# Optimization experiments

Measured on AMD Instinct MI355X. Metric: run time of the kernel, lower is better.

Reference implementation:

```python
import jax, jax.numpy as jnp
import numpy as np

# TT ranks: source list [1,7,7,7,1] interpreted as r_0..r_4 with wraparound r_5 = r_0 = 1
RANKS = [1, 7, 7, 7, 1, 1]
LAYERS = [
    ([7, 4, 4, 4, 7], [8, 8, 8, 8, 4]),   # 3136 -> 16384
    ([8, 8, 8, 8, 4], [8, 8, 8, 4, 4]),   # 16384 -> 8192
    ([8, 8, 8, 4, 4], [8, 8, 4, 4, 4]),   # 8192 -> 4096
    ([8, 8, 4, 4, 4], [8, 4, 4, 4, 4]),   # 4096 -> 2048
    ([8, 4, 4, 4, 4], [10, 1, 1, 1, 1]),  # 2048 -> 10 (out_modes padded with 1s)
]
BATCH = 8192


def tt_linear(x, cores, bias):
    # x: [B, in_features]; cores[i]: [r_i, m_i, n_i, r_{i+1}]
    B = x.shape[0]
    t = x.reshape(B, -1, 1, 1)  # [B, M_remaining, N_done, r]
    for G in cores:
        r0, m, n, r1 = G.shape
        rest = t.shape[1] // m
        t = t.reshape(B, m, rest, t.shape[2], r0)
        # contract current input mode m and incoming rank r0 with the core
        t = jnp.einsum('bmsnp,pmoq->bsnoq', t, G)  # [B, rest, N_done, n, r1]
        t = t.reshape(B, rest, -1, r1)
    return t.reshape(B, -1) + bias  # [B, out_features]


def setup_inputs() -> dict:
    key = jax.random.key(0)
    keys = jax.random.split(key, 32)
    inp = {"x": jax.random.normal(keys[0], (BATCH, 3136), jnp.float32)}
    ki = 1
    for li, (im, om) in enumerate(LAYERS, start=1):
        for ci in range(5):
            shape = (RANKS[ci], im[ci], om[ci], RANKS[ci + 1])
            scale = 1.0 / np.sqrt(im[ci] * RANKS[ci])
            inp[f"l{li}_core{ci}"] = jax.random.normal(keys[ki], shape, jnp.float32) * scale
            ki += 1
        inp[f"l{li}_bias"] = jnp.zeros((int(np.prod(om)),), jnp.float32)
    return inp


def reference(x,
              l1_core0, l1_core1, l1_core2, l1_core3, l1_core4, l1_bias,
              l2_core0, l2_core1, l2_core2, l2_core3, l2_core4, l2_bias,
              l3_core0, l3_core1, l3_core2, l3_core3, l3_core4, l3_bias,
              l4_core0, l4_core1, l4_core2, l4_core3, l4_core4, l4_bias,
              l5_core0, l5_core1, l5_core2, l5_core3, l5_core4, l5_bias):
    h = jax.nn.relu(tt_linear(x, [l1_core0, l1_core1, l1_core2, l1_core3, l1_core4], l1_bias))
    h = jax.nn.relu(tt_linear(h, [l2_core0, l2_core1, l2_core2, l2_core3, l2_core4], l2_bias))
    h = jax.nn.relu(tt_linear(h, [l3_core0, l3_core1, l3_core2, l3_core3, l3_core4], l3_bias))
    h = jax.nn.relu(tt_linear(h, [l4_core0, l4_core1, l4_core2, l4_core3, l4_core4], l4_bias))
    logits = tt_linear(h, [l5_core0, l5_core1, l5_core2, l5_core3, l5_core4], l5_bias)
    return jax.nn.softmax(logits, axis=1)
```

## Files before the change

### kernel.cpp

```cpp
#include <hip/hip_runtime.h>
#include <stdint.h>
#include <stddef.h>

typedef _Float16 f16;
typedef _Float16 f16x8 __attribute__((ext_vector_type(8)));
typedef float    f32x4 __attribute__((ext_vector_type(4)));

#define NB 8192

struct Ptrs {
  const float *G0[5], *G1[5], *G2[5], *G3[5], *bias[5];
  float *T01[5], *T23[5], *biasr[5];
  f16   *WHt[5];
};

__global__ void prep1_kernel(Ptrs p) {
  constexpr int IM[5][5] = {{7,4,4,4,7},{8,8,8,8,4},{8,8,8,4,4},{8,8,4,4,4},{8,4,4,4,4}};
  constexpr int OM[5][5] = {{8,8,8,8,4},{8,8,8,4,4},{8,8,4,4,4},{8,4,4,4,4},{10,1,1,1,1}};
  const int job = blockIdx.x;
  const int tid = threadIdx.x;
  if (job < 5) {
    const int L = job;
    const int m1=IM[L][1], n0=OM[L][0], n1=OM[L][1];
    const int n01 = n0*n1;
    const int cnt = IM[L][0]*m1*n01*7;
    const float* G0 = p.G0[L]; const float* G1 = p.G1[L];
    float* T = p.T01[L];
    for (int e = tid; e < cnt; e += blockDim.x) {
      const int r2  = e % 7;
      const int j01 = (e/7) % n01;
      const int i01 = e / (7*n01);
      const int i0 = i01/m1, i1 = i01 - i0*m1;
      const int j0 = j01/n1, j1 = j01 - j0*n1;
      float s = 0.f;
      for (int r1 = 0; r1 < 7; ++r1)
        s += G0[(i0*n0 + j0)*7 + r1] * G1[((r1*m1 + i1)*n1 + j1)*7 + r2];
      T[e] = s;
    }
  } else if (job < 10) {
    const int L = job - 5;
    const int m2=IM[L][2], m3=IM[L][3], n2=OM[L][2], n3=OM[L][3];
    const int n23 = n2*n3;
    const int cnt = m2*m3*n23*7;
    const float* G2 = p.G2[L]; const float* G3 = p.G3[L];
    float* T = p.T23[L];
    for (int e = tid; e < cnt; e += blockDim.x) {
      const int r2  = e % 7;
      const int j23 = (e/7) % n23;
      const int i23 = e / (7*n23);
      const int i2 = i23/m3, i3 = i23 - i2*m3;
      const int j2 = j23/n3, j3 = j23 - j2*n3;
      float s = 0.f;
      for (int r3 = 0; r3 < 7; ++r3)
        s += G2[((r2*m2 + i2)*n2 + j2)*7 + r3] * G3[(r3*m3 + i3)*n3 + j3];
      T[e] = s;
    }
  } else {
    const int L = job - 10;
    constexpr int OUTF[5] = {16384, 8192, 4096, 2048, 10};
    constexpr int N4[5]   = {4,4,4,4,1};
    const int of = OUTF[L], n4 = N4[L], outH = of / n4;
    const float* b = p.bias[L];
    float* br = p.biasr[L];
    for (int e = tid; e < of; e += blockDim.x) {
      const int j4 = e / outH, jH = e - j4*outH;
      br[e] = b[jH*n4 + j4];
    }
  }
}

__global__ void prep2_kernel(Ptrs p) {
  constexpr int INH[5]  = {448, 4096, 2048, 1024, 512};
  constexpr int M23[5]  = {16, 64, 32, 16, 16};
  constexpr int N23[5]  = {64, 32, 16, 16, 1};
  constexpr int N01[5]  = {64, 64, 64, 32, 10};
  constexpr int BASE[6] = {0, 1835008, 10223616, 12320768, 12845056, 12850176};
  const int total = BASE[5];
  for (int e = blockIdx.x*blockDim.x + threadIdx.x; e < total;
       e += gridDim.x*blockDim.x) {
    int L = 0;
    while (L < 4 && e >= BASE[L+1]) ++L;
    const int le = e - BASE[L];
    const int iH = le % INH[L];
    const int jH = le / INH[L];
    const int i01 = iH / M23[L], i23 = iH - i01*M23[L];
    const int j01 = jH / N23[L], j23 = jH - j01*N23[L];
    const float* a = p.T01[L] + (i01*N01[L] + j01)*7;
    const float* b = p.T23[L] + (i23*N23[L] + j23)*7;
    float s = 0.f;
#pragma unroll
    for (int r = 0; r < 7; ++r) s += a[r]*b[r];
    p.WHt[L][le] = (f16)s;
  }
}

__global__ void stagea_x(const float* __restrict__ x, const float* __restrict__ g4,
                         f16* __restrict__ u, int BC) {
  const int idx = blockIdx.x*blockDim.x + threadIdx.x;
  if (idx >= BC*448) return;
  const int b = idx / 448, c = idx - b*448;
  const float* xr = x + (size_t)b*3136 + c*7;
  float v[7];
#pragma unroll
  for (int i = 0; i < 7; ++i) v[i] = xr[i];
#pragma unroll
  for (int j = 0; j < 4; ++j) {
    float s = 0.f;
#pragma unroll
    for (int i = 0; i < 7; ++i) s += v[i]*g4[i*4+j];
    u[(size_t)(b*4+j)*448 + c] = (f16)s;
  }
}

__global__ void __launch_bounds__(512, 2)
gemm256(const f16* __restrict__ A, const f16* __restrict__ Bt,
        f16* __restrict__ U, const float* __restrict__ biasr,
        const float* __restrict__ g4n,
        int N, int K, int n4n)
{
  __shared__ f16 Ls[2][2][256*64];

  const int tid  = threadIdx.x;
  const int wid  = tid >> 6, lane = tid & 63;
  const int wr   = wid >> 2, wc = wid & 3;
  const int l15  = lane & 15, l4 = lane >> 4, lm = l15 & 7;

  const int nwg = gridDim.x;
  int wg = blockIdx.x;
  if ((nwg & 7) == 0) wg = (wg & 7) * (nwg >> 3) + (wg >> 3);
  const int Nt = N >> 8;
  const int bx = wg / Nt, by = wg - bx * Nt;
  const int m0 = bx << 8, n0 = by << 8;

  const int rr   = tid >> 3;
  const int cs8  = (((tid & 7) ^ (rr & 7)) << 3);
  const int dst0 = tid << 3;

  const int cz0 = ((l4 ^ lm)) << 3;
  const int cz1 = ((4 + l4) ^ lm) << 3;
  const int ax0 = ((wr << 7) + l15) * 64 + cz0;
  const int ax1 = ((wr << 7) + l15) * 64 + cz1;
  const int bx0 = ((wc << 6) + l15) * 64 + cz0;
  const int bx1 = ((wc << 6) + l15) * 64 + cz1;

  f32x4 acc[8][4] = {};
  f16x8 af0[8], bf0[4], af1[8], bf1[4];

  auto stage = [&](int buf, int kt) {
    const f16* gA = A + (size_t)m0 * K + kt;
    const f16* gB = Bt + (size_t)n0 * K + kt;
    f16* dA = &Ls[buf][0][0];
    f16* dB = &Ls[buf][1][0];
#pragma unroll
    for (int q = 0; q < 4; ++q)
      __builtin_amdgcn_global_load_lds(
          (const __attribute__((address_space(1))) void*)(gA + (size_t)(q*64 + rr)*K + cs8),
          (__attribute__((address_space(3))) void*)(dA + q*4096 + dst0), 16, 0, 0);
#pragma unroll
    for (int q = 0; q < 4; ++q)
      __builtin_amdgcn_global_load_lds(
          (const __attribute__((address_space(1))) void*)(gB + (size_t)(q*64 + rr)*K + cs8),
          (__attribute__((address_space(3))) void*)(dB + q*4096 + dst0), 16, 0, 0);
  };

  stage(0, 0);
  asm volatile("s_waitcnt vmcnt(0)" ::: "memory");
  __builtin_amdgcn_s_barrier();
#pragma unroll
  for (int n = 0; n < 4; ++n) bf0[n] = *(const f16x8*)(&Ls[0][1][0] + bx0 + n*1024);
#pragma unroll
  for (int m = 0; m < 8; ++m) af0[m] = *(const f16x8*)(&Ls[0][0][0] + ax0 + m*1024);

  const int nt = K >> 6;
  for (int t = 0; t < nt - 1; ++t) {
    const int cur = t & 1;
    stage(cur ^ 1, (t + 1) << 6);
    __builtin_amdgcn_sched_barrier(0);
    {
      const f16* As = &Ls[cur][0][0];
      const f16* Bs = &Ls[cur][1][0];
#pragma unroll
      for (int n = 0; n < 4; ++n) bf1[n] = *(const f16x8*)(Bs + bx1 + n*1024);
#pragma unroll
      for (int m = 0; m < 8; ++m) af1[m] = *(const f16x8*)(As + ax1 + m*1024);
    }
    __builtin_amdgcn_sched_barrier(0);
    __builtin_amdgcn_s_setprio(1);
#pragma unroll
    for (int m = 0; m < 8; ++m)
#pragma unroll
      for (int n = 0; n < 4; ++n)
        acc[m][n] = __builtin_amdgcn_mfma_f32_16x16x32_f16(af0[m], bf0[n], acc[m][n], 0, 0, 0);
    __builtin_amdgcn_s_setprio(0);
    __builtin_amdgcn_sched_barrier(0);
    asm volatile("s_waitcnt vmcnt(0)" ::: "memory");
    __builtin_amdgcn_s_barrier();
    __builtin_amdgcn_sched_barrier(0);
    {
      const f16* As = &Ls[cur ^ 1][0][0];
      const f16* Bs = &Ls[cur ^ 1][1][0];
#pragma unroll
      for (int n = 0; n < 4; ++n) bf0[n] = *(const f16x8*)(Bs + bx0 + n*1024);
#pragma unroll
      for (int m = 0; m < 8; ++m) af0[m] = *(const f16x8*)(As + ax0 + m*1024);
    }
    __builtin_amdgcn_sched_barrier(0);
    __builtin_amdgcn_s_setprio(1);
#pragma unroll
    for (int m = 0; m < 8; ++m)
#pragma unroll
      for (int n = 0; n < 4; ++n)
        acc[m][n] = __builtin_amdgcn_mfma_f32_16x16x32_f16(af1[m], bf1[n], acc[m][n], 0, 0, 0);
    __builtin_amdgcn_s_setprio(0);
  }
  {
    const int cur = (nt - 1) & 1;
    const f16* As = &Ls[cur][0][0];
    const f16* Bs = &Ls[cur][1][0];
#pragma unroll
    for (int n = 0; n < 4; ++n) bf1[n] = *(const f16x8*)(Bs + bx1 + n*1024);
#pragma unroll
    for (int m = 0; m < 8; ++m) af1[m] = *(const f16x8*)(As + ax1 + m*1024);
    __builtin_amdgcn_s_setprio(1);
#pragma unroll
    for (int m = 0; m < 8; ++m)
#pragma unroll
      for (int n = 0; n < 4; ++n)
        acc[m][n] = __builtin_amdgcn_mfma_f32_16x16x32_f16(af0[m], bf0[n], acc[m][n], 0, 0, 0);
#pragma unroll
    for (int m = 0; m < 8; ++m)
#pragma unroll
      for (int n = 0; n < 4; ++n)
        acc[m][n] = __builtin_amdgcn_mfma_f32_16x16x32_f16(af1[m], bf1[n], acc[m][n], 0, 0, 0);
    __builtin_amdgcn_s_setprio(0);
  }

#pragma unroll
  for (int m = 0; m < 8; ++m) {
    const int rb = m0 + (wr << 7) + (m << 4) + (l4 << 2);
    const int b  = rb >> 2;
#pragma unroll
    for (int n = 0; n < 4; ++n) {
      const int col = n0 + (wc << 6) + (n << 4) + l15;
      float v[4];
#pragma unroll
      for (int r = 0; r < 4; ++r)
        v[r] = fmaxf(acc[m][n][r] + biasr[(size_t)r * N + col], 0.f);
      if (n4n == 4) {
#pragma unroll
        for (int j = 0; j < 4; ++j) {
          float s = v[0]*g4n[j] + v[1]*g4n[4+j] + v[2]*g4n[8+j] + v[3]*g4n[12+j];
          U[(size_t)(b*4 + j) * N + col] = (f16)s;
        }
      } else {
        float s = v[0]*g4n[0] + v[1]*g4n[1] + v[2]*g4n[2] + v[3]*g4n[3];
        U[(size_t)b * N + col] = (f16)s;
      }
    }
  }
}

__global__ void __launch_bounds__(256, 2)
gemm_fused(const f16* __restrict__ A, const f16* __restrict__ Bt,
           f16* __restrict__ U, const float* __restrict__ biasr,
           const float* __restrict__ g4n,
           int N, int K, int n4n)
{
  __shared__ f16 Ls[2][2][128*64];

  const int tid  = threadIdx.x;
  const int wid  = tid >> 6, lane = tid & 63;
  const int wr   = wid >> 1, wc = wid & 1;
  const int l15  = lane & 15, l4 = lane >> 4, lm = l15 & 7;

  const int nwg = gridDim.x;
  int wg = blockIdx.x;
  if ((nwg & 7) == 0) wg = (wg & 7) * (nwg >> 3) + (wg >> 3);
  const int Nt = N >> 7;
  const int bx = wg / Nt, by = wg - bx * Nt;
  const int m0 = bx << 7, n0 = by << 7;

  const int rr   = tid >> 3;
  const int cs8  = (((tid & 7) ^ (rr & 7)) << 3);
  const int dst0 = wid << 9;

  int axoff[2], bxoff[2];
#pragma unroll
  for (int h = 0; h < 2; ++h) {
    const int cz = (((h << 2) + l4) ^ lm) << 3;
    axoff[h] = ((wr << 6) + l15) * 64 + cz;
    bxoff[h] = ((wc << 6) + l15) * 64 + cz;
  }

  f32x4 acc[4][4] = {};

  auto stage = [&](int buf, int kt) {
    const f16* gA = A + (size_t)m0 * K + kt;
    const f16* gB = Bt + (size_t)n0 * K + kt;
    f16* dA = &Ls[buf][0][0];
    f16* dB = &Ls[buf][1][0];
#pragma unroll
    for (int q = 0; q < 4; ++q)
      __builtin_amdgcn_global_load_lds(
          (const __attribute__((address_space(1))) void*)(gA + (size_t)(q*32 + rr)*K + cs8),
          (__attribute__((address_space(3))) void*)(dA + q*2048 + dst0), 16, 0, 0);
#pragma unroll
    for (int q = 0; q < 4; ++q)
      __builtin_amdgcn_global_load_lds(
          (const __attribute__((address_space(1))) void*)(gB + (size_t)(q*32 + rr)*K + cs8),
          (__attribute__((address_space(3))) void*)(dB + q*2048 + dst0), 16, 0, 0);
  };

  stage(0, 0);
  __syncthreads();
  const int nt = K >> 6;
  int cur = 0;
  for (int t = 0; t < nt; ++t) {
    if (t + 1 < nt) stage(cur ^ 1, (t + 1) << 6);
    __builtin_amdgcn_sched_barrier(0);
    const f16* As = &Ls[cur][0][0];
    const f16* Bs = &Ls[cur][1][0];
#pragma unroll
    for (int h = 0; h < 2; ++h) {
      f16x8 af[4], bf[4];
#pragma unroll
      for (int n = 0; n < 4; ++n) bf[n] = *(const f16x8*)(Bs + bxoff[h] + n*1024);
#pragma unroll
      for (int m = 0; m < 4; ++m) af[m] = *(const f16x8*)(As + axoff[h] + m*1024);
      __builtin_amdgcn_s_setprio(1);
#pragma unroll
      for (int m = 0; m < 4; ++m)
#pragma unroll
        for (int n = 0; n < 4; ++n)
          acc[m][n] = __builtin_amdgcn_mfma_f32_16x16x32_f16(af[m], bf[n], acc[m][n], 0, 0, 0);
      __builtin_amdgcn_s_setprio(0);
    }
    __syncthreads();
    cur ^= 1;
  }

#pragma unroll
  for (int m = 0; m < 4; ++m) {
    const int rb = m0 + (wr << 6) + (m << 4) + (l4 << 2);
    const int b  = rb >> 2;
#pragma unroll
    for (int n = 0; n < 4; ++n) {
      const int col = n0 + (wc << 6) + (n << 4) + l15;
      float v[4];
#pragma unroll
      for (int r = 0; r < 4; ++r)
        v[r] = fmaxf(acc[m][n][r] + biasr[(size_t)r * N + col], 0.f);
      if (n4n == 4) {
#pragma unroll
        for (int j = 0; j < 4; ++j) {
          float s = v[0]*g4n[j] + v[1]*g4n[4+j] + v[2]*g4n[8+j] + v[3]*g4n[12+j];
          U[(size_t)(b*4 + j) * N + col] = (f16)s;
        }
      } else {
        float s = v[0]*g4n[0] + v[1]*g4n[1] + v[2]*g4n[2] + v[3]*g4n[3];
        U[(size_t)b * N + col] = (f16)s;
      }
    }
  }
}

__global__ void l5_softmax(const f16* __restrict__ u, const f16* __restrict__ Wt,
                           const float* __restrict__ bias, float* __restrict__ out)
{
  const int wid = threadIdx.x >> 6, lane = threadIdx.x & 63;
  const int row = blockIdx.x*4 + wid;
  float acc[10] = {};
  const f16* ur = u + (size_t)row*512;
#pragma unroll
  for (int t = 0; t < 8; ++t) {
    const float a = (float)ur[t*64 + lane];
#pragma unroll
    for (int j = 0; j < 10; ++j)
      acc[j] += a * (float)Wt[j*512 + t*64 + lane];
  }
#pragma unroll
  for (int j = 0; j < 10; ++j) {
#pragma unroll
    for (int s = 32; s; s >>= 1) acc[j] += __shfl_xor(acc[j], s);
    acc[j] += bias[j];
  }
  float mx = acc[0];
#pragma unroll
  for (int j = 1; j < 10; ++j) mx = fmaxf(mx, acc[j]);
  float sum = 0.f;
#pragma unroll
  for (int j = 0; j < 10; ++j) { acc[j] = __expf(acc[j]-mx); sum += acc[j]; }
  const float inv = 1.f / sum;
  if (lane < 10) out[(size_t)row*10 + lane] = acc[lane]*inv;
}

extern "C" void kernel_launch(void* const* d_in, const int* in_sizes, int n_in,
                              void* d_out, int out_size, void* d_ws, size_t ws_size,
                              hipStream_t stream) {
  (void)in_sizes; (void)n_in; (void)out_size;
  const float* x = (const float*)d_in[0];
  Ptrs p;
  const float* G4[5];
  for (int L = 0; L < 5; ++L) {
    p.G0[L]   = (const float*)d_in[1 + L*6 + 0];
    p.G1[L]   = (const float*)d_in[1 + L*6 + 1];
    p.G2[L]   = (const float*)d_in[1 + L*6 + 2];
    p.G3[L]   = (const float*)d_in[1 + L*6 + 3];
    G4[L]     = (const float*)d_in[1 + L*6 + 4];
    p.bias[L] = (const float*)d_in[1 + L*6 + 5];
  }

  uintptr_t w = (uintptr_t)d_ws;
  auto alloc = [&](size_t bytes) {
    uintptr_t r = w; w += (bytes + 255) & ~(size_t)255; return (void*)r;
  };
  constexpr int  t01sz[5] = {12544, 28672, 28672, 14336, 2240};
  constexpr int  t23sz[5] = {7168, 14336, 3584, 1792, 112};
  constexpr int  brsz[5]  = {16384, 8192, 4096, 2048, 10};
  constexpr long whsz[5]  = {448L*4096, 4096L*2048, 2048L*1024, 1024L*512, 512L*10};
  for (int L = 0; L < 5; ++L) p.T01[L]   = (float*)alloc((size_t)t01sz[L]*4);
  for (int L = 0; L < 5; ++L) p.T23[L]   = (float*)alloc((size_t)t23sz[L]*4);
  for (int L = 0; L < 5; ++L) p.biasr[L] = (float*)alloc((size_t)brsz[L]*4);
  for (int L = 0; L < 5; ++L) p.WHt[L]   = (f16*)alloc((size_t)whsz[L]*2);
  const size_t fixedBytes = (size_t)(w - (uintptr_t)d_ws);

  int BC = 0;
  for (int c = NB; c >= 64; c >>= 1)
    if (fixedBytes + (size_t)c * (16384 + 32768) <= ws_size) { BC = c; break; }
  if (!BC) return;
  f16* bufA = (f16*)alloc((size_t)BC*16384);
  f16* bufB = (f16*)alloc((size_t)BC*32768);

  prep1_kernel<<<15, 256, 0, stream>>>(p);
  prep2_kernel<<<4096, 256, 0, stream>>>(p);

  const int nch = NB / BC;
  const int M   = BC * 4;
  for (int ch = 0; ch < nch; ++ch) {
    const size_t cs = (size_t)ch * BC;
    stagea_x<<<(BC*448 + 255)/256, 256, 0, stream>>>(x + cs*3136, G4[0], bufA, BC);
    gemm256<<<(M/256)*(4096/256), 512, 0, stream>>>(bufA, p.WHt[0], bufB, p.biasr[0],
                                                    G4[1], 4096, 448, 4);
    gemm256<<<(M/256)*(2048/256), 512, 0, stream>>>(bufB, p.WHt[1], bufA, p.biasr[1],
                                                    G4[2], 2048, 4096, 4);
    gemm256<<<(M/256)*(1024/256), 512, 0, stream>>>(bufA, p.WHt[2], bufB, p.biasr[2],
                                                    G4[3], 1024, 2048, 4);
    gemm_fused<<<(M/128)*(512/128), 256, 0, stream>>>(bufB, p.WHt[3], bufA, p.biasr[3],
                                                      G4[4], 512, 1024, 1);
    l5_softmax<<<BC/4, 256, 0, stream>>>(bufA, p.WHt[4], p.biasr[4],
                                         (float*)d_out + cs*10);
  }
}
```

Measured before the change: 940.6 us.

## Software-pipeline LDS fragment loads against MFMA in the GEMM main loop

Restructures the GEMM K-loop so the LDS fragment reads for the second half-tile, and for the next tile's first half, are issued while MFMAs on already-loaded fragments run. Double-buffered register fragments (af0/bf0, af1/bf1) are used, with a peeled prologue and epilogue. `__syncthreads` is replaced by an explicit vmcnt wait plus `s_barrier`, and sched_barriers pin the ordering. This aims to hide LDS read latency behind MFMA issue, at the cost of more VGPRs and tighter reliance on manual wait and barrier placement for correctness.

```diff
diff --git a/kernel.cpp b/kernel.cpp
--- a/kernel.cpp
+++ b/kernel.cpp
@@ -282,17 +282,17 @@
 
   const int rr   = tid >> 3;
   const int cs8  = (((tid & 7) ^ (rr & 7)) << 3);
-  const int dst0 = wid << 9;
-
-  int axoff[2], bxoff[2];
-#pragma unroll
-  for (int h = 0; h < 2; ++h) {
-    const int cz = (((h << 2) + l4) ^ lm) << 3;
-    axoff[h] = ((wr << 6) + l15) * 64 + cz;
-    bxoff[h] = ((wc << 6) + l15) * 64 + cz;
-  }
+  const int dst0 = tid << 3;
+
+  const int cz0 = ((l4 ^ lm)) << 3;
+  const int cz1 = ((4 + l4) ^ lm) << 3;
+  const int ax0 = ((wr << 6) + l15) * 64 + cz0;
+  const int ax1 = ((wr << 6) + l15) * 64 + cz1;
+  const int bx0 = ((wc << 6) + l15) * 64 + cz0;
+  const int bx1 = ((wc << 6) + l15) * 64 + cz1;
 
   f32x4 acc[4][4] = {};
+  f16x8 af0[4], bf0[4], af1[4], bf1[4];
 
   auto stage = [&](int buf, int kt) {
     const f16* gA = A + (size_t)m0 * K + kt;
@@ -312,31 +312,75 @@
   };
 
   stage(0, 0);
-  __syncthreads();
+  asm volatile("s_waitcnt vmcnt(0)" ::: "memory");
+  __builtin_amdgcn_s_barrier();
+#pragma unroll
+  for (int n = 0; n < 4; ++n) bf0[n] = *(const f16x8*)(&Ls[0][1][0] + bx0 + n*1024);
+#pragma unroll
+  for (int m = 0; m < 4; ++m) af0[m] = *(const f16x8*)(&Ls[0][0][0] + ax0 + m*1024);
+
   const int nt = K >> 6;
-  int cur = 0;
-  for (int t = 0; t < nt; ++t) {
-    if (t + 1 < nt) stage(cur ^ 1, (t + 1) << 6);
-    __builtin_amdgcn_sched_barrier(0);
+  for (int t = 0; t < nt - 1; ++t) {
+    const int cur = t & 1;
+    stage(cur ^ 1, (t + 1) << 6);
+    __builtin_amdgcn_sched_barrier(0);
+    {
+      const f16* As = &Ls[cur][0][0];
+      const f16* Bs = &Ls[cur][1][0];
+#pragma unroll
+      for (int n = 0; n < 4; ++n) bf1[n] = *(const f16x8*)(Bs + bx1 + n*1024);
+#pragma unroll
+      for (int m = 0; m < 4; ++m) af1[m] = *(const f16x8*)(As + ax1 + m*1024);
+    }
+    __builtin_amdgcn_sched_barrier(0);
+    __builtin_amdgcn_s_setprio(1);
+#pragma unroll
+    for (int m = 0; m < 4; ++m)
+#pragma unroll
+      for (int n = 0; n < 4; ++n)
+        acc[m][n] = __builtin_amdgcn_mfma_f32_16x16x32_f16(af0[m], bf0[n], acc[m][n], 0, 0, 0);
+    __builtin_amdgcn_s_setprio(0);
+    __builtin_amdgcn_sched_barrier(0);
+    asm volatile("s_waitcnt vmcnt(0)" ::: "memory");
+    __builtin_amdgcn_s_barrier();
+    __builtin_amdgcn_sched_barrier(0);
+    {
+      const f16* As = &Ls[cur ^ 1][0][0];
+      const f16* Bs = &Ls[cur ^ 1][1][0];
+#pragma unroll
+      for (int n = 0; n < 4; ++n) bf0[n] = *(const f16x8*)(Bs + bx0 + n*1024);
+#pragma unroll
+      for (int m = 0; m < 4; ++m) af0[m] = *(const f16x8*)(As + ax0 + m*1024);
+    }
+    __builtin_amdgcn_sched_barrier(0);
+    __builtin_amdgcn_s_setprio(1);
+#pragma unroll
+    for (int m = 0; m < 4; ++m)
+#pragma unroll
+      for (int n = 0; n < 4; ++n)
+        acc[m][n] = __builtin_amdgcn_mfma_f32_16x16x32_f16(af1[m], bf1[n], acc[m][n], 0, 0, 0);
+    __builtin_amdgcn_s_setprio(0);
+  }
+  {
+    const int cur = (nt - 1) & 1;
     const f16* As = &Ls[cur][0][0];
     const f16* Bs = &Ls[cur][1][0];
 #pragma unroll
-    for (int h = 0; h < 2; ++h) {
-      f16x8 af[4], bf[4];
-#pragma unroll
-      for (int n = 0; n < 4; ++n) bf[n] = *(const f16x8*)(Bs + bxoff[h] + n*1024);
-#pragma unroll
-      for (int m = 0; m < 4; ++m) af[m] = *(const f16x8*)(As + axoff[h] + m*1024);
-      __builtin_amdgcn_s_setprio(1);
-#pragma unroll
-      for (int m = 0; m < 4; ++m)
-#pragma unroll
-        for (int n = 0; n < 4; ++n)
-          acc[m][n] = __builtin_amdgcn_mfma_f32_16x16x32_f16(af[m], bf[n], acc[m][n], 0, 0, 0);
-      __builtin_amdgcn_s_setprio(0);
-    }
-    __syncthreads();
-    cur ^= 1;
+    for (int n = 0; n < 4; ++n) bf1[n] = *(const f16x8*)(Bs + bx1 + n*1024);
+#pragma unroll
+    for (int m = 0; m < 4; ++m) af1[m] = *(const f16x8*)(As + ax1 + m*1024);
+    __builtin_amdgcn_s_setprio(1);
+#pragma unroll
+    for (int m = 0; m < 4; ++m)
+#pragma unroll
+      for (int n = 0; n < 4; ++n)
+        acc[m][n] = __builtin_amdgcn_mfma_f32_16x16x32_f16(af0[m], bf0[n], acc[m][n], 0, 0, 0);
+#pragma unroll
+    for (int m = 0; m < 4; ++m)
+#pragma unroll
+      for (int n = 0; n < 4; ++n)
+        acc[m][n] = __builtin_amdgcn_mfma_f32_16x16x32_f16(af1[m], bf1[n], acc[m][n], 0, 0, 0);
+    __builtin_amdgcn_s_setprio(0);
   }
 
 #pragma unroll
```

Result: no change. 952.7 us (+1.3%).
